# Optimization experiments

Measured on AMD Instinct MI355X. Metric: run time of the kernel, lower is better.

The kernel has to match this reference:

```python
import jax, jax.numpy as jnp
import numpy as np

NUM_HEADS = 16
NEG_INF = -1e30


def setup_inputs() -> dict:
    key = jax.random.key(0)
    k1, k2, k3 = jax.random.split(key, 3)
    B, S, D = 2, 2048, 1024
    x = jax.random.normal(k1, (B, S, D), dtype=jnp.float32)
    # torch Linear(D, 3D, bias=False) stored here already transposed: y = x @ w_qkv
    w_qkv = jax.random.normal(k2, (D, 3 * D), dtype=jnp.float32) * 0.02
    w_out = jax.random.normal(k3, (D, D), dtype=jnp.float32) * 0.02
    return {"x": x, "w_qkv": w_qkv, "w_out": w_out}


def reference(x, w_qkv, w_out):
    B, S, D = x.shape
    H = NUM_HEADS
    dh = D // H
    qkv = x @ w_qkv                      # [B, S, 3D]
    q, k, v = jnp.split(qkv, 3, axis=-1)

    def to_heads(t):
        return t.reshape(B, S, H, dh).transpose(0, 2, 1, 3)  # [B, H, S, dh]

    q, k, v = to_heads(q), to_heads(k), to_heads(v)
    scale = jnp.asarray(dh, x.dtype) ** -0.5
    scores = jnp.einsum('bhqd,bhkd->bhqk', q, k) * scale     # [B, H, S, S]
    causal = jnp.tril(jnp.ones((S, S), dtype=bool))
    scores = jnp.where(causal, scores, NEG_INF)
    attn = jax.nn.softmax(scores, axis=-1)
    out = jnp.einsum('bhqk,bhkd->bhqd', attn, v)             # [B, H, S, dh]
    out = out.transpose(0, 2, 1, 3).reshape(B, S, D)
    return out @ w_out
```

## Files before the change

kernel.cpp:

```cpp
#include <hip/hip_runtime.h>

typedef unsigned short u16;
typedef unsigned int u32;

typedef __bf16 bf16x8 __attribute__((ext_vector_type(8)));
typedef _Float16 f16x8 __attribute__((ext_vector_type(8)));
typedef float f32x4 __attribute__((ext_vector_type(4)));

typedef __attribute__((address_space(1))) u32 as1_u32;
typedef __attribute__((address_space(3))) u32 as3_u32;

#define EKF 0.18033688011112042f

__device__ __forceinline__ u16 f2bf(float x) {
  u32 u = __float_as_uint(x);
  u = u + 0x7fffu + ((u >> 16) & 1u);
  return (u16)(u >> 16);
}
__device__ __forceinline__ u32 pack2(float a, float b) {
  return (u32)f2bf(a) | ((u32)f2bf(b) << 16);
}
__device__ __forceinline__ u32 pkf16(float a, float b) {
  return __builtin_bit_cast(u32, __builtin_amdgcn_cvt_pkrtz(a, b));
}
__device__ __forceinline__ u16 f2h(float a) {
  return (u16)(pkf16(a, a) & 0xffffu);
}
__device__ __forceinline__ void gld_lds16(const u16* g, const u16* l) {
  __builtin_amdgcn_global_load_lds((const as1_u32*)g, (as3_u32*)l, 16, 0, 0);
}

__global__ __launch_bounds__(256) void prepass_kernel(const float* __restrict__ x,
                                                      const float* __restrict__ w_qkv,
                                                      const float* __restrict__ w_out,
                                                      u16* __restrict__ xb,
                                                      u16* __restrict__ wqkvT,
                                                      u16* __restrict__ woutT) {
  __shared__ float tile[64][65];
  int bid = blockIdx.x;
  int t = threadIdx.x;
  if (bid < 4096) {
    int i = bid * 256 + t;
    float4 v = ((const float4*)x)[i];
    uint2 r;
    r.x = pack2(v.x, v.y);
    r.y = pack2(v.z, v.w);
    ((uint2*)xb)[i] = r;
    return;
  }
  const float* W;
  u16* WT;
  int K, N, bx, by;
  if (bid < 4096 + 768) {
    int b2 = bid - 4096;
    W = w_qkv; WT = wqkvT; K = 1024; N = 3072; bx = b2 & 15; by = b2 >> 4;
  } else {
    int b2 = bid - 4864;
    W = w_out; WT = woutT; K = 1024; N = 1024; bx = b2 & 15; by = b2 >> 4;
  }
  int k0 = bx * 64, n0 = by * 64;
  int r = t >> 4, c4 = (t & 15) * 4;
#pragma unroll
  for (int i = 0; i < 4; ++i) {
    int row = r + i * 16;
    float4 v = *(const float4*)&W[(size_t)(k0 + row) * N + n0 + c4];
    tile[row][c4 + 0] = v.x; tile[row][c4 + 1] = v.y;
    tile[row][c4 + 2] = v.z; tile[row][c4 + 3] = v.w;
  }
  __syncthreads();
#pragma unroll
  for (int i = 0; i < 4; ++i) {
    int n = r + i * 16;
    uint2 o;
    o.x = pack2(tile[c4 + 0][n], tile[c4 + 1][n]);
    o.y = pack2(tile[c4 + 2][n], tile[c4 + 3][n]);
    *(uint2*)&WT[(size_t)(n0 + n) * K + k0 + c4] = o;
  }
}

__global__ __launch_bounds__(256) void transpose_vt_kernel(const u16* __restrict__ vtmp,
                                                           u16* __restrict__ vt) {
  __shared__ u16 t[64 * 71];
  int j0 = blockIdx.x * 64;
  int bh = blockIdx.y;
  int b = bh >> 4, h = bh & 15;
  int tid = threadIdx.x;
  int r = tid >> 2, cs = (tid & 3) * 16;
  const u16* src = vtmp + (size_t)(b * 2048 + j0 + r) * 1024 + h * 64 + cs;
  uint4 a = ((const uint4*)src)[0];
  uint4 c = ((const uint4*)src)[1];
  u16* dst = &t[r * 71 + cs];
  dst[0] = (u16)a.x; dst[1] = (u16)(a.x >> 16); dst[2] = (u16)a.y; dst[3] = (u16)(a.y >> 16);
  dst[4] = (u16)a.z; dst[5] = (u16)(a.z >> 16); dst[6] = (u16)a.w; dst[7] = (u16)(a.w >> 16);
  dst[8] = (u16)c.x; dst[9] = (u16)(c.x >> 16); dst[10] = (u16)c.y; dst[11] = (u16)(c.y >> 16);
  dst[12] = (u16)c.z; dst[13] = (u16)(c.z >> 16); dst[14] = (u16)c.w; dst[15] = (u16)(c.w >> 16);
  __syncthreads();
  int d = tid >> 2, jseg = (tid & 3) * 16;
  u32 w[8];
#pragma unroll
  for (int i = 0; i < 8; ++i) {
    u32 lo = t[(jseg + 2 * i) * 71 + d];
    u32 hi = t[(jseg + 2 * i + 1) * 71 + d];
    w[i] = lo | (hi << 16);
  }
  u16* out = vt + (size_t)(bh * 64 + d) * 2048 + j0 + jseg;
  ((uint4*)out)[0] = make_uint4(w[0], w[1], w[2], w[3]);
  ((uint4*)out)[1] = make_uint4(w[4], w[5], w[6], w[7]);
}

template <int OUT_MODE, int BN>
__global__ __launch_bounds__(256) void gemm_bt_kernel(const u16* __restrict__ A,
                                                      const u16* __restrict__ BT,
                                                      void* __restrict__ Cv,
                                                      u16* __restrict__ VT,
                                                      int M, int N, int K) {
  const int NF = (BN == 128) ? 4 : 2;
  __shared__ __attribute__((aligned(16))) u16 sA[128 * 32];
  __shared__ __attribute__((aligned(16))) u16 sB[BN * 32];
  const int tid = threadIdx.x;
  const int wave = tid >> 6;
  const int lane = tid & 63;
  const int bm = blockIdx.y * 128;
  const int bn = blockIdx.x * BN;
  const int wm = (wave >> 1) * 64;
  const int wn = (wave & 1) * (BN / 2);
  const int lr = lane & 15;
  const int kg = lane >> 4;

  const int srow = tid >> 2;
  const int scol = (tid & 3) * 8;
  const u16* pa0 = A + (size_t)(bm + srow) * K + scol;
  const u16* pa1 = pa0 + (size_t)64 * K;
  const u16* pb0 = BT + (size_t)(bn + srow) * K + scol;
  const u16* pb1 = pb0 + (size_t)64 * K;
  const u16* la = sA + wave * 512;
  const u16* lb = sB + wave * 512;

  f32x4 acc[4][NF];
#pragma unroll
  for (int i = 0; i < 4; i++)
#pragma unroll
    for (int j = 0; j < NF; j++) {
      f32x4 z = {0.f, 0.f, 0.f, 0.f};
      acc[i][j] = z;
    }

  for (int k0 = 0; k0 < K; k0 += 32) {
    __syncthreads();
    gld_lds16(pa0 + k0, la);
    gld_lds16(pa1 + k0, la + 2048);
    gld_lds16(pb0 + k0, lb);
    if (BN == 128) gld_lds16(pb1 + k0, lb + 2048);
    __syncthreads();
    bf16x8 af[4], bfr[NF];
#pragma unroll
    for (int mi = 0; mi < 4; mi++)
      af[mi] = *(const bf16x8*)(sA + (wm + mi * 16 + lr) * 32 + kg * 8);
#pragma unroll
    for (int ni = 0; ni < NF; ni++)
      bfr[ni] = *(const bf16x8*)(sB + (wn + ni * 16 + lr) * 32 + kg * 8);
#pragma unroll
    for (int mi = 0; mi < 4; mi++)
#pragma unroll
      for (int ni = 0; ni < NF; ni++)
        acc[mi][ni] = __builtin_amdgcn_mfma_f32_16x16x32_bf16(af[mi], bfr[ni], acc[mi][ni], 0, 0, 0);
  }

#pragma unroll
  for (int mi = 0; mi < 4; mi++)
#pragma unroll
    for (int ni = 0; ni < NF; ni++) {
      int c = bn + wn + ni * 16 + lr;
      int r0 = bm + wm + mi * 16 + kg * 4;
      if (OUT_MODE == 0) {
#pragma unroll
        for (int rr = 0; rr < 4; rr++)
          ((float*)Cv)[(size_t)(r0 + rr) * N + c] = acc[mi][ni][rr];
      } else {
        if (c < 1024) {
          u16* qkp = (u16*)Cv;
#pragma unroll
          for (int rr = 0; rr < 4; rr++)
            qkp[(size_t)(r0 + rr) * 2048 + c] = f2bf(acc[mi][ni][rr] * EKF);
        } else if (c < 2048) {
          u16* qkp = (u16*)Cv;
#pragma unroll
          for (int rr = 0; rr < 4; rr++)
            qkp[(size_t)(r0 + rr) * 2048 + c] = f2bf(acc[mi][ni][rr]);
        } else {
          int cc = c - 2048;
#pragma unroll
          for (int rr = 0; rr < 4; rr++)
            VT[(size_t)(r0 + rr) * 1024 + cc] = f2h(acc[mi][ni][rr]);
        }
      }
    }
}

__global__ __launch_bounds__(256, 4) void attn_mfma_kernel(const u16* __restrict__ qk,
                                                           const u16* __restrict__ vt,
                                                           u16* __restrict__ out) {
  __shared__ __attribute__((aligned(16))) u16 sK[2][64 * 64];
  __shared__ __attribute__((aligned(16))) u16 sV[2][64 * 64];
  __shared__ __attribute__((aligned(16))) u16 sP[4][16 * 64];

  const int tid = threadIdx.x;
  const int wave = tid >> 6;
  const int lane = tid & 63;
  const int lr = lane & 15;
  const int kg = lane >> 4;
  const int l7 = lr & 7;

  int idx = blockIdx.x;
  int qi = 31 - (idx >> 5);
  int bh = idx & 31;
  int b = bh >> 4, h = bh & 15;
  int q0 = qi * 64;

  const u16* qbase = qk + (size_t)b * 2048 * 2048 + h * 64;
  const u16* kbase = qbase + 1024;
  const u16* vbase = vt + (size_t)bh * 64 * 2048;
  u16* obase = out + (size_t)b * 2048 * 1024 + h * 64;

  const int sra = wave * 16 + (lane >> 3);
  const int srb = sra + 8;
  const int sc = lane & 7;
  const u32 koffA = (u32)sra * 2048 + (u32)((sc ^ (sra & 7)) * 8);
  const u32 koffB = (u32)srb * 2048 + (u32)((sc ^ (srb & 7)) * 8);
  const u32 ldsA = (wave * 2 + 0) * 512;
  const u32 ldsB = (wave * 2 + 1) * 512;

  const int qcol = q0 + wave * 16 + lr;
  bf16x8 qf0, qf1;
  {
    const u16* qrow = qbase + (size_t)qcol * 2048;
    qf0 = *(const bf16x8*)(qrow + kg * 8);
    qf1 = *(const bf16x8*)(qrow + 32 + kg * 8);
  }

  const u32 ka0 = (u32)(lr * 64 + ((kg ^ l7) * 8));
  const u32 ka1 = (u32)(lr * 64 + (((4 + kg) ^ l7) * 8));
  u16* const sPw = sP[wave];
  const u32 pr0 = (u32)(lr * 64 + (((kg * 2) ^ (l7 << 1)) * 4));
  const u32 pr1 = (u32)(lr * 64 + (((8 + kg * 2) ^ (l7 << 1)) * 4));

  f32x4 oacc[4];
#pragma unroll
  for (int i = 0; i < 4; ++i) {
    f32x4 z = {0.f, 0.f, 0.f, 0.f};
    oacc[i] = z;
  }
  float lsum = 0.f;

  const int nrounds = qi + 1;
  gld_lds16(kbase + koffA, sK[0] + ldsA);
  gld_lds16(kbase + koffB, sK[0] + ldsB);
  gld_lds16(vbase + koffA, sV[0] + ldsA);
  gld_lds16(vbase + koffB, sV[0] + ldsB);
  __syncthreads();

  for (int t = 0; t < nrounds; ++t) {
    if (t + 1 < nrounds) {
      int j1 = (t + 1) * 64;
      u16* dK = sK[(t + 1) & 1];
      u16* dV = sV[(t + 1) & 1];
      gld_lds16(kbase + (size_t)j1 * 2048 + koffA, dK + ldsA);
      gld_lds16(kbase + (size_t)j1 * 2048 + koffB, dK + ldsB);
      gld_lds16(vbase + j1 + koffA, dV + ldsA);
      gld_lds16(vbase + j1 + koffB, dV + ldsB);
    }
    const u16* sKb = sK[t & 1];
    const u16* sVb = sV[t & 1];
    const bool diag = (t == qi);

#pragma unroll
    for (int jt = 0; jt < 4; ++jt) {
      u16* pw = sPw + lr * 64 + (((jt * 4 + kg) ^ (l7 << 1)) * 4);
      if (!diag || jt <= wave) {
        bf16x8 kf0 = *(const bf16x8*)(sKb + jt * 1024 + ka0);
        bf16x8 kf1 = *(const bf16x8*)(sKb + jt * 1024 + ka1);
        f32x4 c = {0.f, 0.f, 0.f, 0.f};
        c = __builtin_amdgcn_mfma_f32_16x16x32_bf16(kf0, qf0, c, 0, 0, 0);
        c = __builtin_amdgcn_mfma_f32_16x16x32_bf16(kf1, qf1, c, 0, 0, 0);
        float p0 = exp2f(c[0]);
        float p1 = exp2f(c[1]);
        float p2 = exp2f(c[2]);
        float p3 = exp2f(c[3]);
        if (diag && jt == wave) {
          int jr = kg * 4;
          p0 = (jr + 0 <= lr) ? p0 : 0.f;
          p1 = (jr + 1 <= lr) ? p1 : 0.f;
          p2 = (jr + 2 <= lr) ? p2 : 0.f;
          p3 = (jr + 3 <= lr) ? p3 : 0.f;
        }
        lsum += (p0 + p1) + (p2 + p3);
        *(uint2*)pw = make_uint2(pkf16(p0, p1), pkf16(p2, p3));
      } else {
        *(uint2*)pw = make_uint2(0u, 0u);
      }
    }

    asm volatile("" ::: "memory");

    f16x8 pf0 = *(const f16x8*)(sPw + pr0);
    f16x8 pf1 = *(const f16x8*)(sPw + pr1);
#pragma unroll
    for (int dt = 0; dt < 4; ++dt) {
      f16x8 vf0 = *(const f16x8*)(sVb + dt * 1024 + ka0);
      f16x8 vf1 = *(const f16x8*)(sVb + dt * 1024 + ka1);
      oacc[dt] = __builtin_amdgcn_mfma_f32_16x16x32_f16(vf0, pf0, oacc[dt], 0, 0, 0);
      oacc[dt] = __builtin_amdgcn_mfma_f32_16x16x32_f16(vf1, pf1, oacc[dt], 0, 0, 0);
    }
    __syncthreads();
  }

  lsum += __shfl_xor(lsum, 16);
  lsum += __shfl_xor(lsum, 32);
  float inv = 1.0f / lsum;

  u16* orow = obase + (size_t)qcol * 1024;
#pragma unroll
  for (int dt = 0; dt < 4; ++dt) {
    uint2 o2 = make_uint2(pack2(oacc[dt][0] * inv, oacc[dt][1] * inv),
                          pack2(oacc[dt][2] * inv, oacc[dt][3] * inv));
    *(uint2*)(orow + dt * 16 + kg * 4) = o2;
  }
}

extern "C" void kernel_launch(void* const* d_in, const int* in_sizes, int n_in,
                              void* d_out, int out_size, void* d_ws, size_t ws_size,
                              hipStream_t stream) {
  const float* x = (const float*)d_in[0];
  const float* w_qkv = (const float*)d_in[1];
  const float* w_out = (const float*)d_in[2];
  float* out = (float*)d_out;

  char* ws = (char*)d_ws;
  u16* xb    = (u16*)(ws);
  u16* wqkvT = (u16*)(ws + (8u << 20));
  u16* woutT = (u16*)(ws + (14u << 20));
  u16* qkb   = (u16*)(ws + (16u << 20));
  u16* vtb   = (u16*)(ws + (32u << 20));
  u16* vtmp  = (u16*)(ws + (40u << 20));
  u16* attn  = (u16*)(ws + (40u << 20));

  prepass_kernel<<<5120, 256, 0, stream>>>(x, w_qkv, w_out, xb, wqkvT, woutT);

  gemm_bt_kernel<2, 128><<<dim3(3072 / 128, 4096 / 128), 256, 0, stream>>>(
      xb, wqkvT, (void*)qkb, vtmp, 4096, 3072, 1024);

  transpose_vt_kernel<<<dim3(32, 32), 256, 0, stream>>>(vtmp, vtb);

  attn_mfma_kernel<<<1024, 256, 0, stream>>>(qkb, vtb, attn);

  gemm_bt_kernel<0, 64><<<dim3(1024 / 64, 4096 / 128), 256, 0, stream>>>(
      attn, woutT, (void*)out, nullptr, 4096, 1024, 1024);
}
```

Baseline: 183.1 us.

## Fuse V transpose into QKV GEMM epilogue and vectorize output stores

```diff
diff --git a/kernel.cpp b/kernel.cpp
--- a/kernel.cpp
+++ b/kernel.cpp
@@ -76,36 +76,6 @@
     o.y = pack2(tile[c4 + 2][n], tile[c4 + 3][n]);
     *(uint2*)&WT[(size_t)(n0 + n) * K + k0 + c4] = o;
   }
-}
-
-__global__ __launch_bounds__(256) void transpose_vt_kernel(const u16* __restrict__ vtmp,
-                                                           u16* __restrict__ vt) {
-  __shared__ u16 t[64 * 71];
-  int j0 = blockIdx.x * 64;
-  int bh = blockIdx.y;
-  int b = bh >> 4, h = bh & 15;
-  int tid = threadIdx.x;
-  int r = tid >> 2, cs = (tid & 3) * 16;
-  const u16* src = vtmp + (size_t)(b * 2048 + j0 + r) * 1024 + h * 64 + cs;
-  uint4 a = ((const uint4*)src)[0];
-  uint4 c = ((const uint4*)src)[1];
-  u16* dst = &t[r * 71 + cs];
-  dst[0] = (u16)a.x; dst[1] = (u16)(a.x >> 16); dst[2] = (u16)a.y; dst[3] = (u16)(a.y >> 16);
-  dst[4] = (u16)a.z; dst[5] = (u16)(a.z >> 16); dst[6] = (u16)a.w; dst[7] = (u16)(a.w >> 16);
-  dst[8] = (u16)c.x; dst[9] = (u16)(c.x >> 16); dst[10] = (u16)c.y; dst[11] = (u16)(c.y >> 16);
-  dst[12] = (u16)c.z; dst[13] = (u16)(c.z >> 16); dst[14] = (u16)c.w; dst[15] = (u16)(c.w >> 16);
-  __syncthreads();
-  int d = tid >> 2, jseg = (tid & 3) * 16;
-  u32 w[8];
-#pragma unroll
-  for (int i = 0; i < 8; ++i) {
-    u32 lo = t[(jseg + 2 * i) * 71 + d];
-    u32 hi = t[(jseg + 2 * i + 1) * 71 + d];
-    w[i] = lo | (hi << 16);
-  }
-  u16* out = vt + (size_t)(bh * 64 + d) * 2048 + j0 + jseg;
-  ((uint4*)out)[0] = make_uint4(w[0], w[1], w[2], w[3]);
-  ((uint4*)out)[1] = make_uint4(w[4], w[5], w[6], w[7]);
 }
 
 template <int OUT_MODE, int BN>
@@ -163,35 +133,34 @@
     for (int mi = 0; mi < 4; mi++)
 #pragma unroll
       for (int ni = 0; ni < NF; ni++)
-        acc[mi][ni] = __builtin_amdgcn_mfma_f32_16x16x32_bf16(af[mi], bfr[ni], acc[mi][ni], 0, 0, 0);
+        acc[mi][ni] = __builtin_amdgcn_mfma_f32_16x16x32_bf16(bfr[ni], af[mi], acc[mi][ni], 0, 0, 0);
   }
 
 #pragma unroll
   for (int mi = 0; mi < 4; mi++)
 #pragma unroll
     for (int ni = 0; ni < NF; ni++) {
-      int c = bn + wn + ni * 16 + lr;
-      int r0 = bm + wm + mi * 16 + kg * 4;
+      int r = bm + wm + mi * 16 + lr;
+      int c0 = bn + wn + ni * 16 + kg * 4;
+      f32x4 a = acc[mi][ni];
       if (OUT_MODE == 0) {
-#pragma unroll
-        for (int rr = 0; rr < 4; rr++)
-          ((float*)Cv)[(size_t)(r0 + rr) * N + c] = acc[mi][ni][rr];
+        float4 o = make_float4(a[0], a[1], a[2], a[3]);
+        *(float4*)&((float*)Cv)[(size_t)r * N + c0] = o;
       } else {
-        if (c < 1024) {
-          u16* qkp = (u16*)Cv;
+        if (c0 < 1024) {
+          uint2 o = make_uint2(pack2(a[0] * EKF, a[1] * EKF), pack2(a[2] * EKF, a[3] * EKF));
+          *(uint2*)&((u16*)Cv)[(size_t)r * 2048 + c0] = o;
+        } else if (c0 < 2048) {
+          uint2 o = make_uint2(pack2(a[0], a[1]), pack2(a[2], a[3]));
+          *(uint2*)&((u16*)Cv)[(size_t)r * 2048 + c0] = o;
+        } else {
+          int cc = c0 - 2048;
+          int bh2 = (r >> 11) * 16 + (cc >> 6);
+          int j = r & 2047;
+          u16* vrow = VT + ((size_t)bh2 * 64 + (cc & 63)) * 2048 + j;
 #pragma unroll
           for (int rr = 0; rr < 4; rr++)
-            qkp[(size_t)(r0 + rr) * 2048 + c] = f2bf(acc[mi][ni][rr] * EKF);
-        } else if (c < 2048) {
-          u16* qkp = (u16*)Cv;
-#pragma unroll
-          for (int rr = 0; rr < 4; rr++)
-            qkp[(size_t)(r0 + rr) * 2048 + c] = f2bf(acc[mi][ni][rr]);
-        } else {
-          int cc = c - 2048;
-#pragma unroll
-          for (int rr = 0; rr < 4; rr++)
-            VT[(size_t)(r0 + rr) * 1024 + cc] = f2h(acc[mi][ni][rr]);
+            vrow[(size_t)rr * 2048] = f2h(a[rr]);
         }
       }
     }
@@ -341,15 +310,12 @@
   u16* woutT = (u16*)(ws + (14u << 20));
   u16* qkb   = (u16*)(ws + (16u << 20));
   u16* vtb   = (u16*)(ws + (32u << 20));
-  u16* vtmp  = (u16*)(ws + (40u << 20));
   u16* attn  = (u16*)(ws + (40u << 20));
 
   prepass_kernel<<<5120, 256, 0, stream>>>(x, w_qkv, w_out, xb, wqkvT, woutT);
 
   gemm_bt_kernel<2, 128><<<dim3(3072 / 128, 4096 / 128), 256, 0, stream>>>(
-      xb, wqkvT, (void*)qkb, vtmp, 4096, 3072, 1024);
-
-  transpose_vt_kernel<<<dim3(32, 32), 256, 0, stream>>>(vtmp, vtb);
+      xb, wqkvT, (void*)qkb, vtb, 4096, 3072, 1024);
 
   attn_mfma_kernel<<<1024, 256, 0, stream>>>(qkb, vtb, attn);
 
```

Result: no change. 184.1 us (+0.5%).
